# Kernel tuning notes

Measured on AMD Instinct MI355X. Metric: run time of the kernel, lower is better.

## Reference

```python
import jax, jax.numpy as jnp
import numpy as np

T, B, D, H = 512, 128, 1024, 1024


def setup_inputs() -> dict:
    key = jax.random.key(0)
    ks = jax.random.split(key, 6)
    obs = jax.random.normal(ks[0], (T, B, D), jnp.float32)
    resets = jax.random.randint(ks[1], (T, B), 0, 2).astype(bool)
    h0 = jax.random.normal(ks[2], (B, H), jnp.float32)
    c0 = jax.random.normal(ks[3], (B, H), jnp.float32)
    s_in = 1.0 / np.sqrt(D)
    s_h = 1.0 / np.sqrt(H)
    # Fused gate weights in flax order (i, f, g, o) along the last axis.
    Wx = jax.random.uniform(ks[4], (D, 4 * H), jnp.float32, -s_in, s_in)
    Wh = jax.random.uniform(ks[5], (H, 4 * H), jnp.float32, -s_h, s_h)
    b = jnp.zeros((4 * H,), jnp.float32)
    return {"obs": obs, "resets": resets, "h0": h0, "c0": c0, "Wx": Wx, "Wh": Wh, "b": b}


def reference(obs, resets, h0, c0, Wx, Wh, b):
    # obs: [T, B, D], resets: [T, B] bool, h0/c0: [B, H]
    def step(carry, xs):
        h, c = carry
        x, r = xs
        m = r[:, None]
        # initialize_carry returns zeros -> reset masking zeroes the state
        h = jnp.where(m, jnp.zeros_like(h), h)
        c = jnp.where(m, jnp.zeros_like(c), c)
        gates = x @ Wx + h @ Wh + b  # [B, 4H]
        i, f, g, o = jnp.split(gates, 4, axis=-1)
        new_c = jax.nn.sigmoid(f) * c + jax.nn.sigmoid(i) * jnp.tanh(g)
        new_h = jax.nn.sigmoid(o) * jnp.tanh(new_c)
        return (new_h, new_c), new_h

    (hT, cT), out = jax.lax.scan(step, (h0, c0), (obs, resets))
    return out, hT, cT
```

## Files before the change

### kernel.cpp

```cpp
#include <hip/hip_runtime.h>
#include <hip/hip_bf16.h>

#define TT 512
#define BB 128
#define DD 1024
#define HH 1024
#define NG 4096
#define KT 2048

using bf8    = __attribute__((ext_vector_type(8))) short;
using f32x2  = __attribute__((ext_vector_type(2))) float;
using f32x4  = __attribute__((ext_vector_type(4))) float;
using f32x16 = __attribute__((ext_vector_type(16))) float;

__device__ __forceinline__ unsigned short f2bf(float f) {
  unsigned int u = __builtin_bit_cast(unsigned int, f);
  u += 0x7fffu + ((u >> 16) & 1u);
  return (unsigned short)(u >> 16);
}
__device__ __forceinline__ float bf2f(unsigned short u) {
  unsigned int x = ((unsigned int)u) << 16;
  return __builtin_bit_cast(float, x);
}
__device__ __forceinline__ float sigm(float x) { return 1.0f / (1.0f + __expf(-x)); }
__device__ __forceinline__ float ftanh(float x) {
  float e = __expf(2.0f * x);
  return 1.0f - 2.0f / (e + 1.0f);
}

#define LBAR() do {                                        \
    __builtin_amdgcn_sched_barrier(0);                     \
    asm volatile("s_waitcnt lgkmcnt(0)" ::: "memory");     \
    __builtin_amdgcn_s_barrier();                          \
    __builtin_amdgcn_sched_barrier(0);                     \
  } while (0)


__global__ void k_detect(const unsigned int* __restrict__ rw, int* __restrict__ flagmode,
                         unsigned int* __restrict__ flags) {
  __shared__ int any;
  if (threadIdx.x == 0) any = 0;
  __syncthreads();
  int loc = 0;
  for (int i = threadIdx.x; i < (TT * BB) / 4; i += blockDim.x)
    if (rw[i] > 1u) loc = 1;
  if (loc) atomicOr(&any, 1);
  __syncthreads();
  if (threadIdx.x == 0) *flagmode = any;
#pragma unroll
  for (int j = 0; j < 4; ++j) flags[threadIdx.x + j * 256] = 1u;
}

__global__ void k_pack(const float* __restrict__ Wx, const float* __restrict__ Wh,
                       unsigned short* __restrict__ Wp) {
  __shared__ unsigned short tile[64][65];
  const int kt = blockIdx.x & 31;
  const int nt = blockIdx.x >> 5;
  const int k0 = kt * 64, n0 = nt * 64;
  const int t = threadIdx.x;
  {
    const int kl = t >> 2;
    const int nl = (t & 3) * 16;
    const int kg = k0 + kl;
    const float* src = (kg < DD) ? (Wx + (size_t)kg * NG + n0 + nl)
                                 : (Wh + (size_t)(kg - DD) * NG + n0 + nl);
#pragma unroll
    for (int j = 0; j < 16; ++j) tile[kl][nl + j] = f2bf(src[j]);
  }
  __syncthreads();
  {
    const int nl = t >> 2;
    const int kl = (t & 3) * 16;
    unsigned short* dst = Wp + (size_t)(n0 + nl) * KT + k0 + kl;
#pragma unroll
    for (int j = 0; j < 16; ++j) dst[j] = tile[kl + j][nl];
  }
}

__global__ void k_initB3(const float* __restrict__ h0, const unsigned char* __restrict__ rB,
                         const int* __restrict__ rI, const int* __restrict__ flagmode,
                         unsigned short* __restrict__ hbufB) {
  const int i = blockIdx.x * 256 + threadIdx.x;
  if (i >= BB * HH) return;
  const int row = i >> 10, hcol = i & 1023;
  const bool r = (*flagmode) ? (rB[row] != 0) : (rI[row] != 0);
  const unsigned short val = r ? (unsigned short)0 : f2bf(h0[i]);
  const int g = row >> 5, rl = row & 31;
  const size_t e = (size_t)g * 32768 + (size_t)(hcol >> 4) * 512
                 + (size_t)((hcol >> 3) & 1) * 256 + (size_t)rl * 8 + (hcol & 7);
  hbufB[e] = val;
}

__global__ void k_cvt(const float* __restrict__ src, unsigned short* __restrict__ dst) {
  size_t i = ((size_t)blockIdx.x * 256 + threadIdx.x) * 8;
  const size_t stride = (size_t)2048 * 256 * 8;
  for (; i < (size_t)TT * BB * DD; i += stride) {
    f32x4 a = *(const f32x4*)(src + i);
    f32x4 c = *(const f32x4*)(src + i + 4);
    uint4 cv;
    asm("v_cvt_pk_bf16_f32 %0, %1, %2" : "=v"(cv.x) : "v"(a[0]), "v"(a[1]));
    asm("v_cvt_pk_bf16_f32 %0, %1, %2" : "=v"(cv.y) : "v"(a[2]), "v"(a[3]));
    asm("v_cvt_pk_bf16_f32 %0, %1, %2" : "=v"(cv.z) : "v"(c[0]), "v"(c[1]));
    asm("v_cvt_pk_bf16_f32 %0, %1, %2" : "=v"(cv.w) : "v"(c[2]), "v"(c[3]));
    *(bf8*)(dst + i) = __builtin_bit_cast(bf8, cv);
  }
}

#define GEMM_SMEM 69632

__global__ void __launch_bounds__(256)
k_gemm(const unsigned short* __restrict__ A, const unsigned short* __restrict__ Bw,
       unsigned short* __restrict__ C) {
  extern __shared__ char gsm[];
  const int tid = threadIdx.x;
  const int w = tid >> 6, l = tid & 63;
  const int l15 = l & 15, lh4 = l >> 4;
  const int wm2 = w >> 1, wn2 = w & 1;
  const int mt = blockIdx.x >> 5, nt = blockIdx.x & 31;
  const size_t m0 = (size_t)mt * 128, n0 = (size_t)nt * 128;

  f32x4 acc[4][4] = {};

  const int srow = l >> 3;
  const int schunk = (l & 7) ^ srow;

  const unsigned short* Ag[4];
  const unsigned short* Bg[4];
#pragma unroll
  for (int i = 0; i < 4; ++i) {
    const int r = w * 32 + i * 8 + srow;
    Ag[i] = A + (m0 + r) * 1024 + schunk * 8;
    Bg[i] = Bw + (n0 + r) * 2048 + schunk * 8;
  }

#define GSTAGE(BUF, KS) do {                                                        \
    const size_t ko_ = (size_t)(KS) * 64;                                           \
    char* base_ = gsm + (BUF) * 32768;                                              \
    _Pragma("unroll")                                                               \
    for (int i_ = 0; i_ < 4; ++i_) {                                                \
      __builtin_amdgcn_global_load_lds(                                             \
        (const __attribute__((address_space(1))) unsigned int*)(Ag[i_] + ko_),      \
        (__attribute__((address_space(3))) unsigned int*)(base_ + (w*32 + i_*8)*128), \
        16, 0, 0);                                                                  \
      __builtin_amdgcn_global_load_lds(                                             \
        (const __attribute__((address_space(1))) unsigned int*)(Bg[i_] + ko_),      \
        (__attribute__((address_space(3))) unsigned int*)(base_ + 16384 + (w*32 + i_*8)*128), \
        16, 0, 0);                                                                  \
    }                                                                               \
  } while (0)

#define GCOMP(BUF) do {                                                             \
    const char* bA_ = gsm + (BUF) * 32768;                                          \
    const char* bB_ = bA_ + 16384;                                                  \
    _Pragma("unroll")                                                               \
    for (int kk_ = 0; kk_ < 2; ++kk_) {                                             \
      bf8 af_[4], bf_[4];                                                           \
      _Pragma("unroll")                                                             \
      for (int mi_ = 0; mi_ < 4; ++mi_) {                                           \
        const int r_ = wm2 * 64 + mi_ * 16 + l15;                                   \
        af_[mi_] = *(const bf8*)(bA_ + r_ * 128 + ((kk_*64 + lh4*16) ^ ((r_ & 7) << 4))); \
      }                                                                             \
      _Pragma("unroll")                                                             \
      for (int ni_ = 0; ni_ < 4; ++ni_) {                                           \
        const int r_ = wn2 * 64 + ni_ * 16 + l15;                                   \
        bf_[ni_] = *(const bf8*)(bB_ + r_ * 128 + ((kk_*64 + lh4*16) ^ ((r_ & 7) << 4))); \
      }                                                                             \
      _Pragma("unroll")                                                             \
      for (int mi_ = 0; mi_ < 4; ++mi_)                                             \
        _Pragma("unroll")                                                           \
        for (int ni_ = 0; ni_ < 4; ++ni_)                                           \
          acc[mi_][ni_] = __builtin_amdgcn_mfma_f32_16x16x32_bf16(                  \
              af_[mi_], bf_[ni_], acc[mi_][ni_], 0, 0, 0);                          \
    }                                                                               \
  } while (0)

  GSTAGE(0, 0);
  asm volatile("s_waitcnt vmcnt(0)" ::: "memory");
  __syncthreads();
#pragma unroll 1
  for (int ks = 0; ks < 16; ++ks) {
    if (ks < 15) GSTAGE((ks + 1) & 1, ks + 1);
    GCOMP(ks & 1);
    if (ks < 15) {
      asm volatile("s_waitcnt vmcnt(0)" ::: "memory");
      __syncthreads();
    }
  }

  __syncthreads();
  float* ct = (float*)(gsm + w * 17408);
#pragma unroll
  for (int mi = 0; mi < 4; ++mi)
#pragma unroll
    for (int ni = 0; ni < 4; ++ni)
#pragma unroll
      for (int q = 0; q < 4; ++q)
        ct[(mi * 16 + lh4 * 4 + q) * 68 + ni * 16 + l15] = acc[mi][ni][q];
#pragma unroll
  for (int i = 0; i < 8; ++i) {
    const int row = i * 8 + (l >> 3);
    const int c8 = (l & 7) * 8;
    f32x4 v0 = *(const f32x4*)(ct + row * 68 + c8);
    f32x4 v1 = *(const f32x4*)(ct + row * 68 + c8 + 4);
    uint4 cv;
    asm("v_cvt_pk_bf16_f32 %0, %1, %2" : "=v"(cv.x) : "v"(v0[0]), "v"(v0[1]));
    asm("v_cvt_pk_bf16_f32 %0, %1, %2" : "=v"(cv.y) : "v"(v0[2]), "v"(v0[3]));
    asm("v_cvt_pk_bf16_f32 %0, %1, %2" : "=v"(cv.z) : "v"(v1[0]), "v"(v1[1]));
    asm("v_cvt_pk_bf16_f32 %0, %1, %2" : "=v"(cv.w) : "v"(v1[2]), "v"(v1[3]));
    *(bf8*)(C + (m0 + wm2 * 64 + row) * 4096 + n0 + wn2 * 64 + c8) =
        __builtin_bit_cast(bf8, cv);
  }
#undef GSTAGE
#undef GCOMP
}

#define HSLOT3 262144

#define HI3(I) asm volatile("global_load_dwordx4 %0, %1, off sc0 sc1" \
    : "=v"(ha[I]) : "v"(hbB + (I) * 1024) : "memory")

#define BRD3(CI, CN) (*(const bf8*)(sm + \
    (size_t)((((CI) * 2 + lhi) * 64 + (CN) * 32 + l31)) * 16))

#define HC3(CI, VM) do {                                                  \
    bf8 nb0, nb1;                                                         \
    if ((CI) < 15) { nb0 = BRD3(kc0 + (CI) + 1, 0); nb1 = BRD3(kc0 + (CI) + 1, 1); } \
    asm volatile("s_waitcnt vmcnt(" #VM ")" ::: "memory");                \
    __builtin_amdgcn_sched_barrier(0);                                    \
    ac0 = __builtin_amdgcn_mfma_f32_32x32x16_bf16(ha[CI], cb0, ac0, 0, 0, 0); \
    ac1 = __builtin_amdgcn_mfma_f32_32x32x16_bf16(ha[CI], cb1, ac1, 0, 0, 0); \
    cb0 = nb0; cb1 = nb1;                                                 \
  } while (0)

#define SCANH4_SMEM 163840
#define TMP4_OFF 131072

__global__ void __launch_bounds__(256)
k_scanh4(const unsigned char* __restrict__ resetsB, const int* __restrict__ resetsI,
         const float* __restrict__ c0, const float* __restrict__ bias,
         const unsigned short* __restrict__ Wp, const unsigned short* __restrict__ gx,
         unsigned short* __restrict__ hbufB, unsigned int* __restrict__ flags,
         const int* __restrict__ flagmode, float* __restrict__ out) {
  extern __shared__ char sm[];

  const int tid = threadIdx.x;
  const int wq  = tid >> 6;
  const int ln  = tid & 63;
  const int l31 = ln & 31;
  const int lhi = ln >> 5;
  const int kc0 = wq * 16;
  const int bid = blockIdx.x;
  const int g   = bid >> 6;
  const int b   = bid & 63;
  const int byteMode = *flagmode;

  {
    const int c = tid >> 2, seg = tid & 3;
    const int n = (c >> 4) * 1024 + b * 16 + (c & 15);
    const unsigned short* src = Wp + (size_t)n * KT + 1024;
#pragma unroll 8
    for (int i = 0; i < 32; ++i) {
      const int k8 = seg * 32 + i;
      bf8 v = *(const bf8*)(src + k8 * 8);
      *(bf8*)(sm + ((size_t)k8 * 64 + c) * 16) = v;
    }
  }

  const int erow = ln & 31;
  const int hcl  = wq * 4 + (ln >> 5) * 2;
  const int grow = g * 32 + erow;
  const int hc   = b * 16 + hcl;

  float ccx = c0[(size_t)grow * HH + hc];
  float ccy = c0[(size_t)grow * HH + hc + 1];
  const float bx0 = bias[0 * HH + hc], by0 = bias[0 * HH + hc + 1];
  const float bx1 = bias[1 * HH + hc], by1 = bias[1 * HH + hc + 1];
  const float bx2 = bias[2 * HH + hc], by2 = bias[2 * HH + hc + 1];
  const float bx3 = bias[3 * HH + hc], by3 = bias[3 * HH + hc + 1];

  const size_t puboff = (size_t)(hc >> 4) * 1024 + (size_t)((hc >> 3) & 1) * 512
                      + (size_t)erow * 16 + (size_t)(hc & 7) * 2;

  const unsigned int* pollp = flags + ((g * 64 + kc0 + (ln >> 2)) << 2) + (ln & 3);

  __syncthreads();

#pragma unroll 1
  for (int t = 0; t < TT; ++t) {
    const unsigned short* gp = gx + ((size_t)t * BB + grow) * 4096 + hc;
    const unsigned int gx0 = *(const unsigned int*)(gp);
    const unsigned int gx1 = *(const unsigned int*)(gp + 1024);
    const unsigned int gx2 = *(const unsigned int*)(gp + 2048);
    const unsigned int gx3 = *(const unsigned int*)(gp + 3072);
    bool rc, rn = false;
    if (byteMode) {
      rc = resetsB[t * BB + grow] != 0;
      if (t + 1 < TT) rn = resetsB[(t + 1) * BB + grow] != 0;
    } else {
      rc = resetsI[t * BB + grow] != 0;
      if (t + 1 < TT) rn = resetsI[(t + 1) * BB + grow] != 0;
    }

    {
      const unsigned int need = (unsigned int)(t + 1);
      while (true) {
        unsigned int v = __hip_atomic_load(pollp, __ATOMIC_RELAXED,
                                           __HIP_MEMORY_SCOPE_AGENT);
        if (__all(v >= need)) break;
        __builtin_amdgcn_s_sleep(1);
      }
    }
    asm volatile("s_waitcnt vmcnt(0)" ::: "memory");
    __builtin_amdgcn_sched_barrier(0);

    f32x16 ac0 = {0.f,0.f,0.f,0.f, 0.f,0.f,0.f,0.f, 0.f,0.f,0.f,0.f, 0.f,0.f,0.f,0.f};
    f32x16 ac1 = {0.f,0.f,0.f,0.f, 0.f,0.f,0.f,0.f, 0.f,0.f,0.f,0.f, 0.f,0.f,0.f,0.f};
    {
      const char* hbB = (const char*)hbufB + (size_t)(t & 1) * HSLOT3
                      + (size_t)g * 65536 + (size_t)kc0 * 1024
                      + (size_t)lhi * 512 + (size_t)l31 * 16;
      bf8 ha[16];
      HI3(0);  HI3(1);  HI3(2);  HI3(3);  HI3(4);  HI3(5);  HI3(6);  HI3(7);
      HI3(8);  HI3(9);  HI3(10); HI3(11); HI3(12); HI3(13); HI3(14); HI3(15);
      bf8 cb0 = BRD3(kc0, 0), cb1 = BRD3(kc0, 1);
      HC3(0, 15);  HC3(1, 14);  HC3(2, 13);  HC3(3, 12);
      HC3(4, 11);  HC3(5, 10);  HC3(6, 9);   HC3(7, 8);
      HC3(8, 7);   HC3(9, 6);   HC3(10, 5);  HC3(11, 4);
      HC3(12, 3);  HC3(13, 2);  HC3(14, 1);  HC3(15, 0);
    }

    {
      float* tw = (float*)(sm + TMP4_OFF) + wq * 2048;
#pragma unroll
      for (int r = 0; r < 16; ++r) {
        const int rowl = (r & 3) + 8 * (r >> 2) + 4 * lhi;
        const int kx = (rowl & 7) << 2;
        tw[rowl * 64 + (l31 ^ kx)]        = ac0[r];
        tw[rowl * 64 + 32 + (l31 ^ kx)]   = ac1[r];
      }
    }
    LBAR();

    f32x2 s0 = {0.f, 0.f}, s1 = {0.f, 0.f}, s2 = {0.f, 0.f}, s3 = {0.f, 0.f};
    {
      const float* tb = (const float*)(sm + TMP4_OFF) + erow * 64;
      const int kx = (erow & 7) << 2;
#pragma unroll
      for (int w2 = 0; w2 < 4; ++w2) {
        const float* p = tb + w2 * 2048;
        s0 += *(const f32x2*)(p + ((hcl)      ^ kx));
        s1 += *(const f32x2*)(p + ((16 + hcl) ^ kx));
        s2 += *(const f32x2*)(p + ((32 + hcl) ^ kx));
        s3 += *(const f32x2*)(p + ((48 + hcl) ^ kx));
      }
    }
    const float i0 = s0[0] + bf2f((unsigned short)(gx0 & 0xffff)) + bx0;
    const float i1 = s0[1] + bf2f((unsigned short)(gx0 >> 16))    + by0;
    const float f0 = s1[0] + bf2f((unsigned short)(gx1 & 0xffff)) + bx1;
    const float f1 = s1[1] + bf2f((unsigned short)(gx1 >> 16))    + by1;
    const float g0 = s2[0] + bf2f((unsigned short)(gx2 & 0xffff)) + bx2;
    const float g1 = s2[1] + bf2f((unsigned short)(gx2 >> 16))    + by2;
    const float o0 = s3[0] + bf2f((unsigned short)(gx3 & 0xffff)) + bx3;
    const float o1 = s3[1] + bf2f((unsigned short)(gx3 >> 16))    + by3;
    const float cox = rc ? 0.f : ccx;
    const float coy = rc ? 0.f : ccy;
    const float ncx = sigm(f0) * cox + sigm(i0) * ftanh(g0);
    const float ncy = sigm(f1) * coy + sigm(i1) * ftanh(g1);
    const float nhx = sigm(o0) * ftanh(ncx);
    const float nhy = sigm(o1) * ftanh(ncy);
    ccx = ncx; ccy = ncy;

    if (t + 1 < TT) {
      const float hx = rn ? 0.f : nhx, hy = rn ? 0.f : nhy;
      unsigned int hp;
      asm("v_cvt_pk_bf16_f32 %0, %1, %2" : "=v"(hp) : "v"(hx), "v"(hy));
      char* dst = (char*)hbufB + (size_t)((t + 1) & 1) * HSLOT3
                + (size_t)g * 65536 + puboff;
      asm volatile("global_store_dword %0, %1, off sc0 sc1" :: "v"(dst), "v"(hp) : "memory");
      asm volatile("s_waitcnt vmcnt(0)" ::: "memory");
      __builtin_amdgcn_sched_barrier(0);
      if (ln == 0) {
        unsigned int* fp = flags + (bid << 2) + wq;
        const unsigned int val = (unsigned int)(t + 2);
        asm volatile("global_store_dword %0, %1, off sc0 sc1" :: "v"(fp), "v"(val) : "memory");
      }
      f32x2 ov = {nhx, nhy};
      *(f32x2*)(out + (size_t)t * BB * HH + (size_t)grow * HH + hc) = ov;
    } else {
      f32x2 ov = {nhx, nhy};
      f32x2 cv2 = {ncx, ncy};
      *(f32x2*)(out + (size_t)t * BB * HH + (size_t)grow * HH + hc) = ov;
      *(f32x2*)(out + (size_t)TT * BB * HH + (size_t)grow * HH + hc) = ov;
      *(f32x2*)(out + (size_t)TT * BB * HH + (size_t)BB * HH + (size_t)grow * HH + hc) = cv2;
    }

    LBAR();
  }
}

#define SCANH3_SMEM 155648
#define TMP3_OFF 131072

__global__ void __launch_bounds__(256)
k_scanh3(const unsigned char* __restrict__ resetsB, const int* __restrict__ resetsI,
         const float* __restrict__ c0, const float* __restrict__ bias,
         const unsigned short* __restrict__ Wp, const unsigned short* __restrict__ gx,
         unsigned short* __restrict__ hbufB, unsigned int* __restrict__ flags,
         const int* __restrict__ flagmode, float* __restrict__ out) {
  extern __shared__ char sm[];
  float* TG = (float*)(sm + TMP3_OFF);

  const int tid = threadIdx.x;
  const int wq  = tid >> 6;
  const int ln  = tid & 63;
  const int l31 = ln & 31;
  const int lhi = ln >> 5;
  const int kc0 = wq * 16;
  const int bid = blockIdx.x;
  const int g   = bid >> 6;
  const int b   = bid & 63;
  const int byteMode = *flagmode;

  {
    const int c = tid >> 2, seg = tid & 3;
    const int n = (c >> 4) * 1024 + b * 16 + (c & 15);
    const unsigned short* src = Wp + (size_t)n * KT + 1024;
#pragma unroll 8
    for (int i = 0; i < 32; ++i) {
      const int k8 = seg * 32 + i;
      bf8 v = *(const bf8*)(src + k8 * 8);
      *(bf8*)(sm + ((size_t)k8 * 64 + c) * 16) = v;
    }
  }

  const int row  = tid >> 3;
  const int jd   = tid & 7;
  const int grow = g * 32 + row;
  const int hc   = b * 16 + jd * 2;

  float ccx = c0[(size_t)grow * HH + hc];
  float ccy = c0[(size_t)grow * HH + hc + 1];
  const float bx0 = bias[0 * HH + hc], by0 = bias[0 * HH + hc + 1];
  const float bx1 = bias[1 * HH + hc], by1 = bias[1 * HH + hc + 1];
  const float bx2 = bias[2 * HH + hc], by2 = bias[2 * HH + hc + 1];
  const float bx3 = bias[3 * HH + hc], by3 = bias[3 * HH + hc + 1];

  const size_t puboff = (size_t)(hc >> 4) * 1024 + (size_t)((hc >> 3) & 1) * 512
                      + (size_t)row * 16 + (size_t)(hc & 7) * 2;

  __syncthreads();

#pragma unroll 1
  for (int t = 0; t < TT; ++t) {
    const unsigned short* gp = gx + ((size_t)t * BB + grow) * 4096 + hc;
    const unsigned int gx0 = *(const unsigned int*)(gp);
    const unsigned int gx1 = *(const unsigned int*)(gp + 1024);
    const unsigned int gx2 = *(const unsigned int*)(gp + 2048);
    const unsigned int gx3 = *(const unsigned int*)(gp + 3072);
    bool rc, rn = false;
    if (byteMode) {
      rc = resetsB[t * BB + grow] != 0;
      if (t + 1 < TT) rn = resetsB[(t + 1) * BB + grow] != 0;
    } else {
      rc = resetsI[t * BB + grow] != 0;
      if (t + 1 < TT) rn = resetsI[(t + 1) * BB + grow] != 0;
    }

    {
      const unsigned int need = (unsigned int)(t + 1);
      const unsigned int* fp = flags + g * 64;
      while (true) {
        unsigned int v = __hip_atomic_load(&fp[ln], __ATOMIC_RELAXED,
                                           __HIP_MEMORY_SCOPE_AGENT);
        if (__all(v >= need)) break;
        __builtin_amdgcn_s_sleep(2);
      }
    }
    asm volatile("s_waitcnt vmcnt(0)" ::: "memory");
    __builtin_amdgcn_sched_barrier(0);

    f32x16 ac0 = {0.f,0.f,0.f,0.f, 0.f,0.f,0.f,0.f, 0.f,0.f,0.f,0.f, 0.f,0.f,0.f,0.f};
    f32x16 ac1 = {0.f,0.f,0.f,0.f, 0.f,0.f,0.f,0.f, 0.f,0.f,0.f,0.f, 0.f,0.f,0.f,0.f};
    {
      const char* hbB = (const char*)hbufB + (size_t)(t & 1) * HSLOT3
                      + (size_t)g * 65536 + (size_t)kc0 * 1024
                      + (size_t)lhi * 512 + (size_t)l31 * 16;
      bf8 ha[16];
      HI3(0);  HI3(1);  HI3(2);  HI3(3);  HI3(4);  HI3(5);  HI3(6);  HI3(7);
      HI3(8);  HI3(9);  HI3(10); HI3(11); HI3(12); HI3(13); HI3(14); HI3(15);
      bf8 cb0 = BRD3(kc0, 0), cb1 = BRD3(kc0, 1);
      HC3(0, 15);  HC3(1, 14);  HC3(2, 13);  HC3(3, 12);
      HC3(4, 11);  HC3(5, 10);  HC3(6, 9);   HC3(7, 8);
      HC3(8, 7);   HC3(9, 6);   HC3(10, 5);  HC3(11, 4);
      HC3(12, 3);  HC3(13, 2);  HC3(14, 1);  HC3(15, 0);
    }

    if (wq > 0) {
      char* tp = sm + TMP3_OFF + (wq - 1) * 8192 + ln * 16;
#pragma unroll
      for (int qd = 0; qd < 4; ++qd) {
        f32x4 v0 = {ac0[qd*4+0], ac0[qd*4+1], ac0[qd*4+2], ac0[qd*4+3]};
        f32x4 v1 = {ac1[qd*4+0], ac1[qd*4+1], ac1[qd*4+2], ac1[qd*4+3]};
        *(f32x4*)(tp + qd * 1024)        = v0;
        *(f32x4*)(tp + 4096 + qd * 1024) = v1;
      }
    }
    __syncthreads();
    if (wq == 0) {
#pragma unroll
      for (int s = 0; s < 3; ++s) {
        const char* tp = sm + TMP3_OFF + s * 8192 + ln * 16;
#pragma unroll
        for (int qd = 0; qd < 4; ++qd) {
          f32x4 v0 = *(const f32x4*)(tp + qd * 1024);
          f32x4 v1 = *(const f32x4*)(tp + 4096 + qd * 1024);
          ac0[qd*4+0] += v0[0]; ac0[qd*4+1] += v0[1];
          ac0[qd*4+2] += v0[2]; ac0[qd*4+3] += v0[3];
          ac1[qd*4+0] += v1[0]; ac1[qd*4+1] += v1[1];
          ac1[qd*4+2] += v1[2]; ac1[qd*4+3] += v1[3];
        }
      }
    }
    __syncthreads();
    if (wq == 0) {
#pragma unroll
      for (int r = 0; r < 16; ++r) {
        const int rowl = (r & 3) + 8 * (r >> 2) + 4 * lhi;
        TG[rowl * 66 + l31]      = ac0[r];
        TG[rowl * 66 + 32 + l31] = ac1[r];
      }
    }
    __syncthreads();

    const float* GLr = TG + row * 66;
    const int hl = jd * 2;
    const float i0 = GLr[ 0 + hl]     + bf2f((unsigned short)(gx0 & 0xffff)) + bx0;
    const float i1 = GLr[ 0 + hl + 1] + bf2f((unsigned short)(gx0 >> 16))    + by0;
    const float f0 = GLr[16 + hl]     + bf2f((unsigned short)(gx1 & 0xffff)) + bx1;
    const float f1 = GLr[16 + hl + 1] + bf2f((unsigned short)(gx1 >> 16))    + by1;
    const float g0 = GLr[32 + hl]     + bf2f((unsigned short)(gx2 & 0xffff)) + bx2;
    const float g1 = GLr[32 + hl + 1] + bf2f((unsigned short)(gx2 >> 16))    + by2;
    const float o0 = GLr[48 + hl]     + bf2f((unsigned short)(gx3 & 0xffff)) + bx3;
    const float o1 = GLr[48 + hl + 1] + bf2f((unsigned short)(gx3 >> 16))    + by3;
    const float cox = rc ? 0.f : ccx;
    const float coy = rc ? 0.f : ccy;
    const float ncx = sigm(f0) * cox + sigm(i0) * ftanh(g0);
    const float ncy = sigm(f1) * coy + sigm(i1) * ftanh(g1);
    const float nhx = sigm(o0) * ftanh(ncx);
    const float nhy = sigm(o1) * ftanh(ncy);
    ccx = ncx; ccy = ncy;

    if (t + 1 < TT) {
      const float hx = rn ? 0.f : nhx, hy = rn ? 0.f : nhy;
      unsigned int hp;
      asm("v_cvt_pk_bf16_f32 %0, %1, %2" : "=v"(hp) : "v"(hx), "v"(hy));
      char* dst = (char*)hbufB + (size_t)((t + 1) & 1) * HSLOT3
                + (size_t)g * 65536 + puboff;
      asm volatile("global_store_dword %0, %1, off sc0 sc1" :: "v"(dst), "v"(hp) : "memory");
      asm volatile("s_waitcnt vmcnt(0)" ::: "memory");
      __syncthreads();
      if (tid == 0) {
        unsigned int* fp = flags + bid;
        const unsigned int val = (unsigned int)(t + 2);
        asm volatile("global_store_dword %0, %1, off sc0 sc1" :: "v"(fp), "v"(val) : "memory");
      }
      float* op = out + (size_t)t * BB * HH + (size_t)grow * HH + hc;
      op[0] = nhx; op[1] = nhy;
    } else {
      float* op = out + (size_t)t * BB * HH + (size_t)grow * HH + hc;
      op[0] = nhx; op[1] = nhy;
      float* hp2 = out + (size_t)TT * BB * HH + (size_t)grow * HH + hc;
      hp2[0] = nhx; hp2[1] = nhy;
      float* cp2 = out + (size_t)TT * BB * HH + (size_t)BB * HH + (size_t)grow * HH + hc;
      cp2[0] = ncx; cp2[1] = ncy;
    }
  }
}


extern "C" void kernel_launch(void* const* d_in, const int* in_sizes, int n_in,
                              void* d_out, int out_size, void* d_ws, size_t ws_size,
                              hipStream_t stream) {
  const float* obs  = (const float*)d_in[0];
  const void*  rst  = d_in[1];
  const float* h0   = (const float*)d_in[2];
  const float* c0   = (const float*)d_in[3];
  const float* Wx   = (const float*)d_in[4];
  const float* Wh   = (const float*)d_in[5];
  const float* bias = (const float*)d_in[6];
  float* out = (float*)d_out;

  char* ws = (char*)d_ws;
  const size_t WP_OFF    = 0;
  const size_t FLAGS_OFF = ((size_t)16 << 20) + ((size_t)512 << 10);
  const size_t HBUFB_OFF = (size_t)17 << 20;
  const size_t OBSBF_OFF = (size_t)24 << 20;
  const size_t GX_OFF    = OBSBF_OFF + ((size_t)128 << 20);

  unsigned short* Wp    = (unsigned short*)(ws + WP_OFF);
  unsigned int*   flags = (unsigned int*)(ws + FLAGS_OFF);
  int*        flagmode  = (int*)(flags + 1024);
  unsigned short* hbufB = (unsigned short*)(ws + HBUFB_OFF);
  unsigned short* obsbf = (unsigned short*)(ws + OBSBF_OFF);
  unsigned short* gxp   = (unsigned short*)(ws + GX_OFF);

  const unsigned char* rB = (const unsigned char*)rst;
  const int* rI = (const int*)rst;

  k_detect<<<1, 256, 0, stream>>>((const unsigned int*)rst, flagmode, flags);
  k_pack<<<dim3((KT / 64) * (NG / 64)), dim3(256), 0, stream>>>(Wx, Wh, Wp);
  k_initB3<<<dim3((BB * HH) / 256), dim3(256), 0, stream>>>(h0, rB, rI, flagmode, hbufB);
  k_cvt<<<dim3(2048), dim3(256), 0, stream>>>(obs, obsbf);
  hipFuncSetAttribute((const void*)k_gemm,
                      hipFuncAttributeMaxDynamicSharedMemorySize, GEMM_SMEM);
  k_gemm<<<dim3((TT * BB / 128) * (NG / 128)), dim3(256), GEMM_SMEM, stream>>>(
      obsbf, Wp, gxp);

  void* args4[] = { (void*)&rB, (void*)&rI, (void*)&c0, (void*)&bias, (void*)&Wp,
                    (void*)&gxp, (void*)&hbufB, (void*)&flags, (void*)&flagmode,
                    (void*)&out };
  bool ok = hipFuncSetAttribute((const void*)k_scanh4,
                hipFuncAttributeMaxDynamicSharedMemorySize, SCANH4_SMEM) == hipSuccess;
  if (ok)
    ok = hipLaunchCooperativeKernel((const void*)k_scanh4, dim3(256), dim3(256),
                                    args4, SCANH4_SMEM, stream) == hipSuccess;
  if (!ok) {
    (void)hipGetLastError();
    hipFuncSetAttribute((const void*)k_scanh3,
                        hipFuncAttributeMaxDynamicSharedMemorySize, SCANH3_SMEM);
    hipLaunchCooperativeKernel((const void*)k_scanh3, dim3(256), dim3(256),
                               args4, SCANH3_SMEM, stream);
  }
}
```

Measured before the change: 2.758 ms.

## Drop k_scanh4 path, swizzle GEMM block order, relax scan wait

Removes the k_scanh4 kernel, which used per-wave flags, and always launches k_scanh3 with per-block flags, so only 256 flags are initialised. The GEMM block index is swizzled so that consecutive blocks spread across M tiles, which changes the L2 reuse pattern for the weight and activation tiles. In k_scanh3 the s_waitcnt vmcnt(0) after the flag poll is replaced by a plain compiler barrier. That removes a stall, but it could let the gx and reset loads still be in flight when the later inline-asm MFMA code uses them, and the inline waits may not account for them.

After: 2.720 ms. About the same (-1.4%).

```diff
diff --git a/kernel.cpp b/kernel.cpp
--- a/kernel.cpp
+++ b/kernel.cpp
@@ -9,7 +9,6 @@
 #define KT 2048
 
 using bf8    = __attribute__((ext_vector_type(8))) short;
-using f32x2  = __attribute__((ext_vector_type(2))) float;
 using f32x4  = __attribute__((ext_vector_type(4))) float;
 using f32x16 = __attribute__((ext_vector_type(16))) float;
 
@@ -28,13 +27,6 @@
   return 1.0f - 2.0f / (e + 1.0f);
 }
 
-#define LBAR() do {                                        \
-    __builtin_amdgcn_sched_barrier(0);                     \
-    asm volatile("s_waitcnt lgkmcnt(0)" ::: "memory");     \
-    __builtin_amdgcn_s_barrier();                          \
-    __builtin_amdgcn_sched_barrier(0);                     \
-  } while (0)
-
 
 __global__ void k_detect(const unsigned int* __restrict__ rw, int* __restrict__ flagmode,
                          unsigned int* __restrict__ flags) {
@@ -47,8 +39,7 @@
   if (loc) atomicOr(&any, 1);
   __syncthreads();
   if (threadIdx.x == 0) *flagmode = any;
-#pragma unroll
-  for (int j = 0; j < 4; ++j) flags[threadIdx.x + j * 256] = 1u;
+  flags[threadIdx.x] = 1u;
 }
 
 __global__ void k_pack(const float* __restrict__ Wx, const float* __restrict__ Wh,
@@ -116,7 +107,9 @@
   const int w = tid >> 6, l = tid & 63;
   const int l15 = l & 15, lh4 = l >> 4;
   const int wm2 = w >> 1, wn2 = w & 1;
-  const int mt = blockIdx.x >> 5, nt = blockIdx.x & 31;
+  const int bid0 = blockIdx.x;
+  const int swz = (bid0 & 7) * 2048 + (bid0 >> 3);
+  const int mt = swz >> 5, nt = swz & 31;
   const size_t m0 = (size_t)mt * 128, n0 = (size_t)nt * 128;
 
   f32x4 acc[4][4] = {};
@@ -214,6 +207,8 @@
 #undef GCOMP
 }
 
+#define SCANH3_SMEM 155648
+#define TMP3_OFF 131072
 #define HSLOT3 262144
 
 #define HI3(I) asm volatile("global_load_dwordx4 %0, %1, off sc0 sc1" \
@@ -232,16 +227,14 @@
     cb0 = nb0; cb1 = nb1;                                                 \
   } while (0)
 
-#define SCANH4_SMEM 163840
-#define TMP4_OFF 131072
-
 __global__ void __launch_bounds__(256)
-k_scanh4(const unsigned char* __restrict__ resetsB, const int* __restrict__ resetsI,
+k_scanh3(const unsigned char* __restrict__ resetsB, const int* __restrict__ resetsI,
          const float* __restrict__ c0, const float* __restrict__ bias,
          const unsigned short* __restrict__ Wp, const unsigned short* __restrict__ gx,
          unsigned short* __restrict__ hbufB, unsigned int* __restrict__ flags,
          const int* __restrict__ flagmode, float* __restrict__ out) {
   extern __shared__ char sm[];
+  float* TG = (float*)(sm + TMP3_OFF);
 
   const int tid = threadIdx.x;
   const int wq  = tid >> 6;
@@ -266,10 +259,10 @@
     }
   }
 
-  const int erow = ln & 31;
-  const int hcl  = wq * 4 + (ln >> 5) * 2;
-  const int grow = g * 32 + erow;
-  const int hc   = b * 16 + hcl;
+  const int row  = tid >> 3;
+  const int jd   = tid & 7;
+  const int grow = g * 32 + row;
+  const int hc   = b * 16 + jd * 2;
 
   float ccx = c0[(size_t)grow * HH + hc];
   float ccy = c0[(size_t)grow * HH + hc + 1];
@@ -279,9 +272,7 @@
   const float bx3 = bias[3 * HH + hc], by3 = bias[3 * HH + hc + 1];
 
   const size_t puboff = (size_t)(hc >> 4) * 1024 + (size_t)((hc >> 3) & 1) * 512
-                      + (size_t)erow * 16 + (size_t)(hc & 7) * 2;
-
-  const unsigned int* pollp = flags + ((g * 64 + kc0 + (ln >> 2)) << 2) + (ln & 3);
+                      + (size_t)row * 16 + (size_t)(hc & 7) * 2;
 
   __syncthreads();
 
@@ -303,171 +294,6 @@
 
     {
       const unsigned int need = (unsigned int)(t + 1);
-      while (true) {
-        unsigned int v = __hip_atomic_load(pollp, __ATOMIC_RELAXED,
-                                           __HIP_MEMORY_SCOPE_AGENT);
-        if (__all(v >= need)) break;
-        __builtin_amdgcn_s_sleep(1);
-      }
-    }
-    asm volatile("s_waitcnt vmcnt(0)" ::: "memory");
-    __builtin_amdgcn_sched_barrier(0);
-
-    f32x16 ac0 = {0.f,0.f,0.f,0.f, 0.f,0.f,0.f,0.f, 0.f,0.f,0.f,0.f, 0.f,0.f,0.f,0.f};
-    f32x16 ac1 = {0.f,0.f,0.f,0.f, 0.f,0.f,0.f,0.f, 0.f,0.f,0.f,0.f, 0.f,0.f,0.f,0.f};
-    {
-      const char* hbB = (const char*)hbufB + (size_t)(t & 1) * HSLOT3
-                      + (size_t)g * 65536 + (size_t)kc0 * 1024
-                      + (size_t)lhi * 512 + (size_t)l31 * 16;
-      bf8 ha[16];
-      HI3(0);  HI3(1);  HI3(2);  HI3(3);  HI3(4);  HI3(5);  HI3(6);  HI3(7);
-      HI3(8);  HI3(9);  HI3(10); HI3(11); HI3(12); HI3(13); HI3(14); HI3(15);
-      bf8 cb0 = BRD3(kc0, 0), cb1 = BRD3(kc0, 1);
-      HC3(0, 15);  HC3(1, 14);  HC3(2, 13);  HC3(3, 12);
-      HC3(4, 11);  HC3(5, 10);  HC3(6, 9);   HC3(7, 8);
-      HC3(8, 7);   HC3(9, 6);   HC3(10, 5);  HC3(11, 4);
-      HC3(12, 3);  HC3(13, 2);  HC3(14, 1);  HC3(15, 0);
-    }
-
-    {
-      float* tw = (float*)(sm + TMP4_OFF) + wq * 2048;
-#pragma unroll
-      for (int r = 0; r < 16; ++r) {
-        const int rowl = (r & 3) + 8 * (r >> 2) + 4 * lhi;
-        const int kx = (rowl & 7) << 2;
-        tw[rowl * 64 + (l31 ^ kx)]        = ac0[r];
-        tw[rowl * 64 + 32 + (l31 ^ kx)]   = ac1[r];
-      }
-    }
-    LBAR();
-
-    f32x2 s0 = {0.f, 0.f}, s1 = {0.f, 0.f}, s2 = {0.f, 0.f}, s3 = {0.f, 0.f};
-    {
-      const float* tb = (const float*)(sm + TMP4_OFF) + erow * 64;
-      const int kx = (erow & 7) << 2;
-#pragma unroll
-      for (int w2 = 0; w2 < 4; ++w2) {
-        const float* p = tb + w2 * 2048;
-        s0 += *(const f32x2*)(p + ((hcl)      ^ kx));
-        s1 += *(const f32x2*)(p + ((16 + hcl) ^ kx));
-        s2 += *(const f32x2*)(p + ((32 + hcl) ^ kx));
-        s3 += *(const f32x2*)(p + ((48 + hcl) ^ kx));
-      }
-    }
-    const float i0 = s0[0] + bf2f((unsigned short)(gx0 & 0xffff)) + bx0;
-    const float i1 = s0[1] + bf2f((unsigned short)(gx0 >> 16))    + by0;
-    const float f0 = s1[0] + bf2f((unsigned short)(gx1 & 0xffff)) + bx1;
-    const float f1 = s1[1] + bf2f((unsigned short)(gx1 >> 16))    + by1;
-    const float g0 = s2[0] + bf2f((unsigned short)(gx2 & 0xffff)) + bx2;
-    const float g1 = s2[1] + bf2f((unsigned short)(gx2 >> 16))    + by2;
-    const float o0 = s3[0] + bf2f((unsigned short)(gx3 & 0xffff)) + bx3;
-    const float o1 = s3[1] + bf2f((unsigned short)(gx3 >> 16))    + by3;
-    const float cox = rc ? 0.f : ccx;
-    const float coy = rc ? 0.f : ccy;
-    const float ncx = sigm(f0) * cox + sigm(i0) * ftanh(g0);
-    const float ncy = sigm(f1) * coy + sigm(i1) * ftanh(g1);
-    const float nhx = sigm(o0) * ftanh(ncx);
-    const float nhy = sigm(o1) * ftanh(ncy);
-    ccx = ncx; ccy = ncy;
-
-    if (t + 1 < TT) {
-      const float hx = rn ? 0.f : nhx, hy = rn ? 0.f : nhy;
-      unsigned int hp;
-      asm("v_cvt_pk_bf16_f32 %0, %1, %2" : "=v"(hp) : "v"(hx), "v"(hy));
-      char* dst = (char*)hbufB + (size_t)((t + 1) & 1) * HSLOT3
-                + (size_t)g * 65536 + puboff;
-      asm volatile("global_store_dword %0, %1, off sc0 sc1" :: "v"(dst), "v"(hp) : "memory");
-      asm volatile("s_waitcnt vmcnt(0)" ::: "memory");
-      __builtin_amdgcn_sched_barrier(0);
-      if (ln == 0) {
-        unsigned int* fp = flags + (bid << 2) + wq;
-        const unsigned int val = (unsigned int)(t + 2);
-        asm volatile("global_store_dword %0, %1, off sc0 sc1" :: "v"(fp), "v"(val) : "memory");
-      }
-      f32x2 ov = {nhx, nhy};
-      *(f32x2*)(out + (size_t)t * BB * HH + (size_t)grow * HH + hc) = ov;
-    } else {
-      f32x2 ov = {nhx, nhy};
-      f32x2 cv2 = {ncx, ncy};
-      *(f32x2*)(out + (size_t)t * BB * HH + (size_t)grow * HH + hc) = ov;
-      *(f32x2*)(out + (size_t)TT * BB * HH + (size_t)grow * HH + hc) = ov;
-      *(f32x2*)(out + (size_t)TT * BB * HH + (size_t)BB * HH + (size_t)grow * HH + hc) = cv2;
-    }
-
-    LBAR();
-  }
-}
-
-#define SCANH3_SMEM 155648
-#define TMP3_OFF 131072
-
-__global__ void __launch_bounds__(256)
-k_scanh3(const unsigned char* __restrict__ resetsB, const int* __restrict__ resetsI,
-         const float* __restrict__ c0, const float* __restrict__ bias,
-         const unsigned short* __restrict__ Wp, const unsigned short* __restrict__ gx,
-         unsigned short* __restrict__ hbufB, unsigned int* __restrict__ flags,
-         const int* __restrict__ flagmode, float* __restrict__ out) {
-  extern __shared__ char sm[];
-  float* TG = (float*)(sm + TMP3_OFF);
-
-  const int tid = threadIdx.x;
-  const int wq  = tid >> 6;
-  const int ln  = tid & 63;
-  const int l31 = ln & 31;
-  const int lhi = ln >> 5;
-  const int kc0 = wq * 16;
-  const int bid = blockIdx.x;
-  const int g   = bid >> 6;
-  const int b   = bid & 63;
-  const int byteMode = *flagmode;
-
-  {
-    const int c = tid >> 2, seg = tid & 3;
-    const int n = (c >> 4) * 1024 + b * 16 + (c & 15);
-    const unsigned short* src = Wp + (size_t)n * KT + 1024;
-#pragma unroll 8
-    for (int i = 0; i < 32; ++i) {
-      const int k8 = seg * 32 + i;
-      bf8 v = *(const bf8*)(src + k8 * 8);
-      *(bf8*)(sm + ((size_t)k8 * 64 + c) * 16) = v;
-    }
-  }
-
-  const int row  = tid >> 3;
-  const int jd   = tid & 7;
-  const int grow = g * 32 + row;
-  const int hc   = b * 16 + jd * 2;
-
-  float ccx = c0[(size_t)grow * HH + hc];
-  float ccy = c0[(size_t)grow * HH + hc + 1];
-  const float bx0 = bias[0 * HH + hc], by0 = bias[0 * HH + hc + 1];
-  const float bx1 = bias[1 * HH + hc], by1 = bias[1 * HH + hc + 1];
-  const float bx2 = bias[2 * HH + hc], by2 = bias[2 * HH + hc + 1];
-  const float bx3 = bias[3 * HH + hc], by3 = bias[3 * HH + hc + 1];
-
-  const size_t puboff = (size_t)(hc >> 4) * 1024 + (size_t)((hc >> 3) & 1) * 512
-                      + (size_t)row * 16 + (size_t)(hc & 7) * 2;
-
-  __syncthreads();
-
-#pragma unroll 1
-  for (int t = 0; t < TT; ++t) {
-    const unsigned short* gp = gx + ((size_t)t * BB + grow) * 4096 + hc;
-    const unsigned int gx0 = *(const unsigned int*)(gp);
-    const unsigned int gx1 = *(const unsigned int*)(gp + 1024);
-    const unsigned int gx2 = *(const unsigned int*)(gp + 2048);
-    const unsigned int gx3 = *(const unsigned int*)(gp + 3072);
-    bool rc, rn = false;
-    if (byteMode) {
-      rc = resetsB[t * BB + grow] != 0;
-      if (t + 1 < TT) rn = resetsB[(t + 1) * BB + grow] != 0;
-    } else {
-      rc = resetsI[t * BB + grow] != 0;
-      if (t + 1 < TT) rn = resetsI[(t + 1) * BB + grow] != 0;
-    }
-
-    {
-      const unsigned int need = (unsigned int)(t + 1);
       const unsigned int* fp = flags + g * 64;
       while (true) {
         unsigned int v = __hip_atomic_load(&fp[ln], __ATOMIC_RELAXED,
@@ -476,7 +302,7 @@
         __builtin_amdgcn_s_sleep(2);
       }
     }
-    asm volatile("s_waitcnt vmcnt(0)" ::: "memory");
+    asm volatile("" ::: "memory");
     __builtin_amdgcn_sched_barrier(0);
 
     f32x16 ac0 = {0.f,0.f,0.f,0.f, 0.f,0.f,0.f,0.f, 0.f,0.f,0.f,0.f, 0.f,0.f,0.f,0.f};
@@ -616,19 +442,11 @@
   k_gemm<<<dim3((TT * BB / 128) * (NG / 128)), dim3(256), GEMM_SMEM, stream>>>(
       obsbf, Wp, gxp);
 
-  void* args4[] = { (void*)&rB, (void*)&rI, (void*)&c0, (void*)&bias, (void*)&Wp,
+  hipFuncSetAttribute((const void*)k_scanh3,
+                      hipFuncAttributeMaxDynamicSharedMemorySize, SCANH3_SMEM);
+  void* args3[] = { (void*)&rB, (void*)&rI, (void*)&c0, (void*)&bias, (void*)&Wp,
                     (void*)&gxp, (void*)&hbufB, (void*)&flags, (void*)&flagmode,
                     (void*)&out };
-  bool ok = hipFuncSetAttribute((const void*)k_scanh4,
-                hipFuncAttributeMaxDynamicSharedMemorySize, SCANH4_SMEM) == hipSuccess;
-  if (ok)
-    ok = hipLaunchCooperativeKernel((const void*)k_scanh4, dim3(256), dim3(256),
-                                    args4, SCANH4_SMEM, stream) == hipSuccess;
-  if (!ok) {
-    (void)hipGetLastError();
-    hipFuncSetAttribute((const void*)k_scanh3,
-                        hipFuncAttributeMaxDynamicSharedMemorySize, SCANH3_SMEM);
-    hipLaunchCooperativeKernel((const void*)k_scanh3, dim3(256), dim3(256),
-                               args4, SCANH3_SMEM, stream);
-  }
-}
+  hipLaunchCooperativeKernel((const void*)k_scanh3, dim3(256), dim3(256), args3,
+                             SCANH3_SMEM, stream);
+}
```
